# Optimization experiments

Hardware: AMD Instinct MI355X
Metric: run time of the kernel (lower is better)

## Reference

```python
import jax, jax.numpy as jnp
import numpy as np

EPS = 1e-8
UNTANH = 0.5                       # hp UNTANH (blend factor, assumed)
BUNTANH_SCALE = (2.0 + 2.0 ** 0.5) ** 0.5  # sqrt(2 + sqrt(2)) from source
C_MOMENT = 0.99                    # hp c_moment
A_VARIANCE = 0.02                  # hp a_variance
SINKHORN_ITERS = 8


def rms_norm(x, axes):
    ms = jnp.mean(x * x, axis=axes, keepdims=True)
    return x * jax.lax.rsqrt(ms + EPS)


def buntanh(x):
    # blended un-tanh: untanh * identity + (1-untanh) * tanh, rescaled
    return BUNTANH_SCALE * (UNTANH * x + (1.0 - UNTANH) * jnp.tanh(x))


def sinkhorn_knopp(A, n_iter=SINKHORN_ITERS):
    A = jnp.maximum(A, 0.0) + EPS
    def body(A, _):
        A = A / jnp.sum(A, axis=-1, keepdims=True)  # row normalize
        A = A / jnp.sum(A, axis=-2, keepdims=True)  # col normalize
        return A, None
    A, _ = jax.lax.scan(body, A, None, length=n_iter)
    return A


def setup_inputs() -> dict:
    key = jax.random.key(0)
    ks = jax.random.split(key, 8)
    B, N, D, IN_DIM = 4, 1024, 128, 8192
    inv_sqrt_d = 1.0 / np.sqrt(D)
    return {
        "state": jax.random.normal(ks[0], (B, N, D), jnp.float32) * 0.1,
        "output": jax.random.normal(ks[1], (B, N, D), jnp.float32) * 0.1,
        "w1": jax.random.normal(ks[2], (B, N, D, D), jnp.float32) * inv_sqrt_d,
        "w2": jax.random.normal(ks[3], (B, N, D, D), jnp.float32) * inv_sqrt_d,
        "w3": jax.random.normal(ks[4], (B, N, D, D), jnp.float32) * inv_sqrt_d,
        "A_ema": jax.random.normal(ks[5], (B, N, N), jnp.float32) * 0.01,
        "env_input": jax.random.normal(ks[6], (B, IN_DIM), jnp.float32),
        "noise": jax.random.normal(ks[7], (B, N, D), jnp.float32),
    }


def reference(state, output, w1, w2, w3, A_ema, env_input, noise):
    B, N, D = state.shape
    input_dim = env_input.shape[1]
    num_in = -(-input_dim // D)  # ceil

    # first-call mask/EMA adjustment (num_input_nodes change branch)
    A_mask = jnp.ones((N, N), dtype=state.dtype).at[:num_in, :].set(0.0)
    A_ema = A_ema.at[:, num_in, :num_in].add(3.0 / num_in)

    # per-node batched small GEMMs + custom activation
    Q = buntanh(jnp.einsum('bnd,bndk->bnk', state, w3))
    K = buntanh(jnp.einsum('bnd,bndk->bnk', state, w2))
    prediction = buntanh(jnp.einsum('bnd,bndk->bnk', state, w1))

    # QK^T adjacency, rms-normed over full [N,N]
    raw_A = jnp.einsum('bnk,bmk->bnm', Q, K) / jnp.sqrt(jnp.asarray(D, state.dtype))
    raw_A = rms_norm(raw_A, (-2, -1))

    # EMA (non-first step) + input-node masking
    new_A_ema = (A_ema * C_MOMENT + raw_A * (1.0 - C_MOMENT)) * A_mask

    # doubly-stochastic projection, thresholded sparsification, re-project
    dsA = sinkhorn_knopp(new_A_ema)
    baseline = 1.0 / (N + 1.0)
    sparse_A = jnp.where(dsA > baseline, dsA, 0.0)
    A = sinkhorn_knopp(sparse_A) * A_mask

    # boredom noise scaled by variance deficit (torch var is unbiased)
    var = jnp.var(A, axis=(-2, -1), keepdims=True, ddof=1)
    vd = jax.nn.relu(A_VARIANCE - var)
    V = output + vd * noise

    # message passing + softsign, overwrite input-node rows with env input
    target = jax.nn.soft_sign(jnp.einsum('bnm,bmd->bnd', A, V))
    pad = num_in * D - input_dim
    env = jnp.pad(env_input, ((0, 0), (0, pad))).reshape(B, num_in, D)
    target = target.at[:, :num_in, :].set(env)

    out = jnp.concatenate([target, prediction], axis=-1)  # [B,N,2D]
    return out, A
```

## Files before the change

kernel.cpp:

```cpp
#include <hip/hip_runtime.h>
#include <math.h>

#define NB 4
#define NN 1024
#define ND 128
#define NUM_IN 64
#define F_EPS 1e-8f
#define BT_SCALE 1.8477590650225735f
#define INV_SQRT_D 0.08838834764831844f
#define BASELINE (1.0f/1025.0f)
#define OUT_STRIDE 256
#define A_OFF 1048576

__device__ __forceinline__ float buntanh_f(float x) {
    return BT_SCALE * (0.5f * x + 0.5f * tanhf(x));
}
__device__ __forceinline__ float wave_sum(float v) {
    #pragma unroll
    for (int off = 32; off > 0; off >>= 1) v += __shfl_xor(v, off, 64);
    return v;
}
__device__ __forceinline__ float bflo(unsigned u) { return __uint_as_float(u << 16); }
__device__ __forceinline__ float bfhi(unsigned u) { return __uint_as_float(u & 0xffff0000u); }
__device__ __forceinline__ unsigned bf_rne(float f) {
    unsigned x = __float_as_uint(f);
    return (x + 0x7fffu + ((x >> 16) & 1u)) >> 16;
}
__device__ __forceinline__ unsigned bf_pack(float lo, float hi) {
    return bf_rne(lo) | (bf_rne(hi) << 16);
}

typedef float f32x4 __attribute__((ext_vector_type(4)));
__device__ __forceinline__ float4 ntload4(const float4* p) {
    f32x4 v = __builtin_nontemporal_load((const f32x4*)p);
    return make_float4(v.x, v.y, v.z, v.w);
}

__global__ __launch_bounds__(256, 6) void qkp_kernel(
    const float* __restrict__ state,
    const float* __restrict__ w1,
    const float* __restrict__ w2,
    const float* __restrict__ w3,
    float* __restrict__ dout,
    float* __restrict__ Qg,
    float* __restrict__ Kg)
{
    const int blk = blockIdx.x;
    const int node = ((blk & 7) << 9) | (blk >> 3);

    __shared__ float s_state[ND];
    __shared__ float4 red[3][8][32];

    const int t = threadIdx.x;
    if (t < 32) ((float4*)s_state)[t] =
        ((const float4*)(state + ((size_t)node << 7)))[t];
    __syncthreads();

    const int g = t >> 5, m = t & 31;

    auto do_mat = [&](const float* wbase, int q) {
        const float4* w4 = (const float4*)(wbase + ((size_t)node << 14));
        float4 wv[8];
        float4 acc = make_float4(0.f, 0.f, 0.f, 0.f);
        #pragma unroll
        for (int i = 0; i < 8; ++i) wv[i] = ntload4(&w4[i*256 + t]);
        #pragma unroll
        for (int i = 0; i < 8; ++i) {
            const float s = s_state[i*8 + g];
            acc.x += s*wv[i].x; acc.y += s*wv[i].y;
            acc.z += s*wv[i].z; acc.w += s*wv[i].w;
        }
        #pragma unroll
        for (int i = 0; i < 8; ++i) wv[i] = ntload4(&w4[(8+i)*256 + t]);
        #pragma unroll
        for (int i = 0; i < 8; ++i) {
            const float s = s_state[(8+i)*8 + g];
            acc.x += s*wv[i].x; acc.y += s*wv[i].y;
            acc.z += s*wv[i].z; acc.w += s*wv[i].w;
        }
        red[q][g][m] = acc;
    };
    do_mat(w1, 0);
    do_mat(w2, 1);
    do_mat(w3, 2);
    __syncthreads();

    if (t < 96) {
        const int q = t >> 5, mm = t & 31;
        float4 o = red[q][0][mm];
        #pragma unroll
        for (int gg = 1; gg < 8; ++gg) {
            const float4 r = red[q][gg][mm];
            o.x += r.x; o.y += r.y; o.z += r.z; o.w += r.w;
        }
        o.x = buntanh_f(o.x); o.y = buntanh_f(o.y);
        o.z = buntanh_f(o.z); o.w = buntanh_f(o.w);
        if (q == 0) {
            *(float4*)(dout + (size_t)node * OUT_STRIDE + ND + 4*mm) = o;
        } else {
            float* base = (q == 1) ? Kg : Qg;
            *(float4*)(base + ((size_t)node << 7) + 4*mm) = o;
        }
    }
}

__global__ __launch_bounds__(256) void qk2_kernel(
    const float* __restrict__ Qg, const float* __restrict__ Kg,
    unsigned* __restrict__ rawbf, float* __restrict__ reds)
{
    const int b = blockIdx.x >> 10;
    const int tile = blockIdx.x & 1023;
    const int tr = tile >> 5, tc = tile & 31;

    __shared__ float Qs[32][132];
    __shared__ float Ks[32][136];
    __shared__ float wr4[4];

    const int t = threadIdx.x;
    for (int i = t; i < 1024; i += 256) {
        const int r = i >> 5, q = i & 31;
        *(float4*)&Qs[r][q*4] = *(const float4*)(Qg + (((size_t)(b*NN + tr*32 + r)) << 7) + q*4);
        *(float4*)&Ks[r][q*4] = *(const float4*)(Kg + (((size_t)(b*NN + tc*32 + r)) << 7) + q*4);
    }
    __syncthreads();

    const int ty = t >> 4;
    const int tx = t & 15;
    float a00=0.f, a01=0.f, a10=0.f, a11=0.f;
    #pragma unroll
    for (int dq = 0; dq < 32; ++dq) {
        const float4 q0 = *(const float4*)&Qs[ty][dq*4];
        const float4 q1 = *(const float4*)&Qs[ty+16][dq*4];
        const float4 k0 = *(const float4*)&Ks[2*tx][dq*4];
        const float4 k1 = *(const float4*)&Ks[2*tx+1][dq*4];
        a00 += q0.x*k0.x + q0.y*k0.y + q0.z*k0.z + q0.w*k0.w;
        a01 += q0.x*k1.x + q0.y*k1.y + q0.z*k1.z + q0.w*k1.w;
        a10 += q1.x*k0.x + q1.y*k0.y + q1.z*k0.z + q1.w*k0.w;
        a11 += q1.x*k1.x + q1.y*k1.y + q1.z*k1.z + q1.w*k1.w;
    }
    a00 *= INV_SQRT_D; a01 *= INV_SQRT_D; a10 *= INV_SQRT_D; a11 *= INV_SQRT_D;

    unsigned* r0p = rawbf + (((size_t)(b*NN + tr*32 + ty)) << 9) + tc*16;
    unsigned* r1p = rawbf + (((size_t)(b*NN + tr*32 + ty + 16)) << 9) + tc*16;
    r0p[tx] = bf_pack(a00, a01);
    r1p[tx] = bf_pack(a10, a11);

    float ssq = a00*a00 + a01*a01 + a10*a10 + a11*a11;
    ssq = wave_sum(ssq);
    if ((t & 63) == 0) wr4[t >> 6] = ssq;
    __syncthreads();
    if (t == 0) atomicAdd(&reds[b], wr4[0]+wr4[1]+wr4[2]+wr4[3]);
}

__global__ __launch_bounds__(256) void emaT_kernel(
    const unsigned* __restrict__ rawbf, const float* __restrict__ A_ema,
    const float* __restrict__ reds,
    unsigned* __restrict__ M0, unsigned* __restrict__ M0T,
    float* __restrict__ SR)
{
    const int b = blockIdx.x >> 8;
    const int tile = blockIdx.x & 255;
    const int tr = tile >> 4, tc = tile & 15;
    const int R0 = tr << 6, C0 = tc << 6;

    __shared__ float st[64][65];
    __shared__ float s_part[64][5];

    const int t = threadIdx.x;
    const int r = t >> 2, q = t & 3;
    const int row = R0 + r;
    const float scale = rsqrtf(reds[b] * (1.0f/1048576.0f) + F_EPS);

    const unsigned* rawrow = rawbf + (((size_t)(b*NN + row)) << 9) + tc*8*4;
    const uint4 u0 = ((const uint4*)rawrow)[q*2];
    const uint4 u1 = ((const uint4*)rawrow)[q*2 + 1];
    float rv[16];
    rv[0]=bflo(u0.x); rv[1]=bfhi(u0.x); rv[2]=bflo(u0.y); rv[3]=bfhi(u0.y);
    rv[4]=bflo(u0.z); rv[5]=bfhi(u0.z); rv[6]=bflo(u0.w); rv[7]=bfhi(u0.w);
    rv[8]=bflo(u1.x); rv[9]=bfhi(u1.x); rv[10]=bflo(u1.y); rv[11]=bfhi(u1.y);
    rv[12]=bflo(u1.z); rv[13]=bfhi(u1.z); rv[14]=bflo(u1.w); rv[15]=bfhi(u1.w);

    const float* emarow = A_ema + (((size_t)(b*NN + row)) << 10) + C0 + q*16;
    float s = 0.f;
    #pragma unroll
    for (int j = 0; j < 4; ++j) {
        const float4 e = ((const float4*)emarow)[j];
        float ev[4] = {e.x, e.y, e.z, e.w};
        #pragma unroll
        for (int k = 0; k < 4; ++k) {
            const int e_idx = j*4 + k;
            const int c = C0 + q*16 + e_idx;
            float em = ev[k];
            if (row == NUM_IN && c < NUM_IN) em += 3.0f / NUM_IN;
            float v = em * 0.99f + rv[e_idx] * scale * 0.01f;
            if (row < NUM_IN) v = 0.f;
            v = fmaxf(v, 0.f) + F_EPS;
            rv[e_idx] = v;
            st[r][q*16 + e_idx] = v;
            s += v;
        }
    }
    s_part[r][q] = s;

    unsigned* m0row = M0 + (((size_t)(b*NN + row)) << 9) + tc*8*4;
    uint4 o0, o1;
    o0.x = bf_pack(rv[0],rv[1]);  o0.y = bf_pack(rv[2],rv[3]);
    o0.z = bf_pack(rv[4],rv[5]);  o0.w = bf_pack(rv[6],rv[7]);
    o1.x = bf_pack(rv[8],rv[9]);  o1.y = bf_pack(rv[10],rv[11]);
    o1.z = bf_pack(rv[12],rv[13]); o1.w = bf_pack(rv[14],rv[15]);
    ((uint4*)m0row)[q*2]     = o0;
    ((uint4*)m0row)[q*2 + 1] = o1;
    __syncthreads();

    if (t < 64) {
        const float rs = s_part[t][0] + s_part[t][1] + s_part[t][2] + s_part[t][3];
        atomicAdd(&SR[b*NN + R0 + t], rs);
    }

    const int cT = t >> 2;
    float tv[16];
    #pragma unroll
    for (int k = 0; k < 16; ++k) tv[k] = st[q*16 + k][cT];
    uint4 w0, w1;
    w0.x = bf_pack(tv[0],tv[1]);  w0.y = bf_pack(tv[2],tv[3]);
    w0.z = bf_pack(tv[4],tv[5]);  w0.w = bf_pack(tv[6],tv[7]);
    w1.x = bf_pack(tv[8],tv[9]);  w1.y = bf_pack(tv[10],tv[11]);
    w1.z = bf_pack(tv[12],tv[13]); w1.w = bf_pack(tv[14],tv[15]);
    unsigned* mtrow = M0T + (((size_t)(b*NN + C0 + cT)) << 9) + tr*8*4;
    ((uint4*)mtrow)[q*2]     = w0;
    ((uint4*)mtrow)[q*2 + 1] = w1;
}

template<bool INV_IN>
__global__ __launch_bounds__(256) void mv_kernel(
    const unsigned* __restrict__ Abf, const float* __restrict__ x,
    float* __restrict__ y)
{
    const int blk = blockIdx.x;
    const int lp  = ((blk & 7) << 5) | (blk >> 3);
    const int b   = lp >> 6;
    const int r0  = (lp & 63) << 4;
    const int t = threadIdx.x;
    const int w = t >> 6, l = t & 63;

    const float4* xb = (const float4*)(x + (b << 10));
    float4 x0 = xb[2*l], x1 = xb[2*l+1], x2 = xb[128+2*l], x3 = xb[129+2*l];
    if (INV_IN) {
        x0.x=1.f/x0.x; x0.y=1.f/x0.y; x0.z=1.f/x0.z; x0.w=1.f/x0.w;
        x1.x=1.f/x1.x; x1.y=1.f/x1.y; x1.z=1.f/x1.z; x1.w=1.f/x1.w;
        x2.x=1.f/x2.x; x2.y=1.f/x2.y; x2.z=1.f/x2.z; x2.w=1.f/x2.w;
        x3.x=1.f/x3.x; x3.y=1.f/x3.y; x3.z=1.f/x3.z; x3.w=1.f/x3.w;
    }

    #pragma unroll
    for (int r = 0; r < 4; ++r) {
        const int row = r0 + (w << 2) + r;
        const unsigned* rp = Abf + (((size_t)((b << 10) + row)) << 9);
        const uint4 v0 = ((const uint4*)rp)[l];
        const uint4 v1 = ((const uint4*)rp)[64 + l];
        float a = bflo(v0.x)*x0.x + bfhi(v0.x)*x0.y
                + bflo(v0.y)*x0.z + bfhi(v0.y)*x0.w
                + bflo(v0.z)*x1.x + bfhi(v0.z)*x1.y
                + bflo(v0.w)*x1.z + bfhi(v0.w)*x1.w
                + bflo(v1.x)*x2.x + bfhi(v1.x)*x2.y
                + bflo(v1.y)*x2.z + bfhi(v1.y)*x2.w
                + bflo(v1.z)*x3.x + bfhi(v1.z)*x3.y
                + bflo(v1.w)*x3.z + bfhi(v1.w)*x3.w;
        a = wave_sum(a);
        if (l == 0) y[(b << 10) + row] = 1.0f / a;
    }
}

__global__ __launch_bounds__(256) void thresh_kernel(
    const unsigned* __restrict__ M0, const unsigned* __restrict__ M0T,
    const float* __restrict__ r8, const float* __restrict__ c8,
    unsigned* __restrict__ A1, unsigned* __restrict__ A1T,
    float* __restrict__ SR2)
{
    const int t = threadIdx.x;
    const int b = blockIdx.x >> 6;
    const int g0 = (blockIdx.x & 63) << 4;
    const int w = t >> 6, l = t & 63;
    const bool doA1 = (w < 2);
    const int wr = doA1 ? w : (w - 2);
    const unsigned* src = doA1 ? M0 : M0T;
    unsigned*       dst = doA1 ? A1 : A1T;
    const float* rowS = doA1 ? r8 : c8;
    const float* colS = doA1 ? c8 : r8;

    const float4* cb = (const float4*)(colS + (b << 10));
    const float4 c0 = cb[2*l], c1 = cb[2*l+1], c2 = cb[128+2*l], c3 = cb[129+2*l];
    const float cm[16] = {c0.x,c0.y,c0.z,c0.w, c1.x,c1.y,c1.z,c1.w,
                          c2.x,c2.y,c2.z,c2.w, c3.x,c3.y,c3.z,c3.w};

    for (int rr = 0; rr < 8; ++rr) {
        const int row = g0 + wr*8 + rr;
        const float ri = rowS[(b << 10) + row];
        const unsigned* rp = src + (((size_t)(b*NN + row)) << 9);
        const uint4 v0 = ((const uint4*)rp)[l];
        const uint4 v1 = ((const uint4*)rp)[64 + l];
        float e[16];
        e[0]=bflo(v0.x); e[1]=bfhi(v0.x); e[2]=bflo(v0.y); e[3]=bfhi(v0.y);
        e[4]=bflo(v0.z); e[5]=bfhi(v0.z); e[6]=bflo(v0.w); e[7]=bfhi(v0.w);
        e[8]=bflo(v1.x); e[9]=bfhi(v1.x); e[10]=bflo(v1.y); e[11]=bfhi(v1.y);
        e[12]=bflo(v1.z); e[13]=bfhi(v1.z); e[14]=bflo(v1.w); e[15]=bfhi(v1.w);
        float s = 0.f;
        #pragma unroll
        for (int j = 0; j < 16; ++j) {
            const float d = e[j] * ri * cm[j];
            e[j] = (d > BASELINE ? d : 0.f) + F_EPS;
            s += e[j];
        }
        uint4 o0, o1;
        o0.x = bf_pack(e[0],e[1]);  o0.y = bf_pack(e[2],e[3]);
        o0.z = bf_pack(e[4],e[5]);  o0.w = bf_pack(e[6],e[7]);
        o1.x = bf_pack(e[8],e[9]);  o1.y = bf_pack(e[10],e[11]);
        o1.z = bf_pack(e[12],e[13]); o1.w = bf_pack(e[14],e[15]);
        unsigned* op = dst + (((size_t)(b*NN + row)) << 9);
        ((uint4*)op)[l] = o0;
        ((uint4*)op)[64 + l] = o1;
        if (doA1) {
            s = wave_sum(s);
            if (l == 0) SR2[b*NN + row] = s;
        }
    }
}

__global__ __launch_bounds__(256) void fin_kernel(
    const unsigned* __restrict__ A1, const float* __restrict__ r8,
    const float* __restrict__ c8, float* __restrict__ reds,
    float* __restrict__ dout)
{
    __shared__ float wred[8];
    const int t = threadIdx.x;
    const int b = blockIdx.x >> 6;
    const int g0 = (blockIdx.x & 63) << 4;
    const int w = t >> 6, l = t & 63;

    const float4* cb = (const float4*)(c8 + (b << 10));
    const float4 c0 = cb[2*l], c1 = cb[2*l+1], c2 = cb[128+2*l], c3 = cb[129+2*l];
    const float cm[16] = {c0.x,c0.y,c0.z,c0.w, c1.x,c1.y,c1.z,c1.w,
                          c2.x,c2.y,c2.z,c2.w, c3.x,c3.y,c3.z,c3.w};

    float s1 = 0.f, s2 = 0.f;
    for (int rr = 0; rr < 4; ++rr) {
        const int row = g0 + w*4 + rr;
        float* Arow = dout + A_OFF + (((size_t)(b*NN + row)) << 10);
        if (row < NUM_IN) {
            const float4 z = make_float4(0.f,0.f,0.f,0.f);
            ((float4*)Arow)[2*l] = z;       ((float4*)Arow)[2*l+1] = z;
            ((float4*)Arow)[128+2*l] = z;   ((float4*)Arow)[129+2*l] = z;
        } else {
            const float ri = r8[(b << 10) + row];
            const unsigned* rp = A1 + (((size_t)(b*NN + row)) << 9);
            const uint4 v0 = ((const uint4*)rp)[l];
            const uint4 v1 = ((const uint4*)rp)[64 + l];
            float e[16];
            e[0]=bflo(v0.x); e[1]=bfhi(v0.x); e[2]=bflo(v0.y); e[3]=bfhi(v0.y);
            e[4]=bflo(v0.z); e[5]=bfhi(v0.z); e[6]=bflo(v0.w); e[7]=bfhi(v0.w);
            e[8]=bflo(v1.x); e[9]=bfhi(v1.x); e[10]=bflo(v1.y); e[11]=bfhi(v1.y);
            e[12]=bflo(v1.z); e[13]=bfhi(v1.z); e[14]=bflo(v1.w); e[15]=bfhi(v1.w);
            #pragma unroll
            for (int j = 0; j < 16; ++j) {
                e[j] = e[j] * ri * cm[j];
                s1 += e[j]; s2 += e[j]*e[j];
            }
            ((float4*)Arow)[2*l]     = make_float4(e[0],e[1],e[2],e[3]);
            ((float4*)Arow)[2*l+1]   = make_float4(e[4],e[5],e[6],e[7]);
            ((float4*)Arow)[128+2*l] = make_float4(e[8],e[9],e[10],e[11]);
            ((float4*)Arow)[129+2*l] = make_float4(e[12],e[13],e[14],e[15]);
        }
    }
    s1 = wave_sum(s1); s2 = wave_sum(s2);
    if (l == 0) { wred[w] = s1; wred[4 + w] = s2; }
    __syncthreads();
    if (t == 0) {
        atomicAdd(&reds[4 + b], wred[0]+wred[1]+wred[2]+wred[3]);
        atomicAdd(&reds[8 + b], wred[4]+wred[5]+wred[6]+wred[7]);
    }
}

__global__ __launch_bounds__(256) void vbuild_kernel(
    const float* __restrict__ outp, const float* __restrict__ noise,
    const float* __restrict__ reds, float* __restrict__ V)
{
    const int i = blockIdx.x * 256 + threadIdx.x;
    const int b = i >> 15;
    const float Mn = 1048576.f;
    const float S1 = reds[4 + b], S2 = reds[8 + b];
    const float var = (S2 - S1*S1/Mn) / (Mn - 1.f);
    const float vd = fmaxf(0.02f - var, 0.f);
    const float4 o = ((const float4*)outp)[i];
    const float4 n = ((const float4*)noise)[i];
    ((float4*)V)[i] = make_float4(o.x + vd*n.x, o.y + vd*n.y,
                                  o.z + vd*n.z, o.w + vd*n.w);
}

__global__ __launch_bounds__(256) void av_kernel(
    const float* __restrict__ A,
    const float* __restrict__ V,
    const float* __restrict__ env,
    float* __restrict__ dout)
{
    const int b = blockIdx.x >> 5;
    const int rb = blockIdx.x & 31;
    const int r0 = rb << 5;
    const int t = threadIdx.x;

    if (r0 < NUM_IN) {
        for (int i = t; i < 32 * ND; i += 256) {
            const int r = i >> 7, d = i & 127;
            dout[((size_t)(b*NN + r0 + r)) * OUT_STRIDE + d] =
                env[(size_t)b * 8192 + (size_t)(r0 + r) * ND + d];
        }
        return;
    }

    __shared__ float As[32][64];
    const int d = t & 127, rg = t >> 7;
    float acc[16];
    #pragma unroll
    for (int k = 0; k < 16; ++k) acc[k] = 0.f;
    const float* Vb = V + (size_t)b * (NN * ND) + d;

    for (int mc = 0; mc < 16; ++mc) {
        #pragma unroll
        for (int j = 0; j < 2; ++j) {
            const int f = 2*t + j, r = f >> 4, c4 = f & 15;
            *(float4*)&As[r][c4*4] =
                *(const float4*)(A + (((size_t)(b*NN + r0 + r)) << 10) + mc*64 + c4*4);
        }
        __syncthreads();
        #pragma unroll 4
        for (int mm4 = 0; mm4 < 16; ++mm4) {
            const float vv0 = Vb[(size_t)(mc*64 + mm4*4 + 0) * ND];
            const float vv1 = Vb[(size_t)(mc*64 + mm4*4 + 1) * ND];
            const float vv2 = Vb[(size_t)(mc*64 + mm4*4 + 2) * ND];
            const float vv3 = Vb[(size_t)(mc*64 + mm4*4 + 3) * ND];
            #pragma unroll
            for (int k = 0; k < 16; ++k) {
                const float4 a = *(const float4*)&As[rg*16 + k][mm4*4];
                acc[k] += a.x*vv0 + a.y*vv1 + a.z*vv2 + a.w*vv3;
            }
        }
        __syncthreads();
    }
    #pragma unroll
    for (int k = 0; k < 16; ++k) {
        const float o = acc[k];
        dout[((size_t)(b*NN + r0 + rg*16 + k)) * OUT_STRIDE + d] = o / (1.f + fabsf(o));
    }
}

extern "C" void kernel_launch(void* const* d_in, const int* in_sizes, int n_in,
                              void* d_out, int out_size, void* d_ws, size_t ws_size,
                              hipStream_t stream)
{
    (void)in_sizes; (void)n_in; (void)out_size; (void)ws_size;
    const float* state = (const float*)d_in[0];
    const float* outp  = (const float*)d_in[1];
    const float* w1    = (const float*)d_in[2];
    const float* w2    = (const float*)d_in[3];
    const float* w3    = (const float*)d_in[4];
    const float* A_ema = (const float*)d_in[5];
    const float* env   = (const float*)d_in[6];
    const float* noise = (const float*)d_in[7];
    float* dout = (float*)d_out;

    unsigned* M0  = (unsigned*)(dout + A_OFF);
    unsigned* M0T = M0 + 2097152;

    float*    Qg   = (float*)d_ws;
    float*    Kg   = Qg + 524288;
    float*    Vg   = Kg + 524288;
    unsigned* raw  = (unsigned*)(Vg + 524288);
    unsigned* A1   = raw;
    unsigned* A1T  = raw + 2097152;
    float*    SR1  = (float*)(A1T + 2097152);
    float*    reds = SR1 + 4096;
    float*    SC1  = reds + 16;
    float*    SR2  = SC1 + 4096;
    float*    SC2  = SR2 + 4096;
    float*    RV1  = SC2 + 4096;
    float*    RV2  = RV1 + 4096;

    hipMemsetAsync(SR1, 0, (4096 + 16) * sizeof(float), stream);

    qkp_kernel<<<dim3(NB*NN), dim3(256), 0, stream>>>(
        state, w1, w2, w3, dout, Qg, Kg);

    qk2_kernel<<<dim3(NB*1024), dim3(256), 0, stream>>>(Qg, Kg, raw, reds);

    emaT_kernel<<<dim3(NB*256), dim3(256), 0, stream>>>(
        raw, A_ema, reds, M0, M0T, SR1);

    mv_kernel<true ><<<dim3(256), dim3(256), 0, stream>>>(M0T, SR1, SC1);
    for (int k = 1; k < 15; ++k) {
        if (k & 1)
            mv_kernel<false><<<dim3(256), dim3(256), 0, stream>>>(M0, SC1, RV1);
        else
            mv_kernel<false><<<dim3(256), dim3(256), 0, stream>>>(M0T, RV1, SC1);
    }

    thresh_kernel<<<dim3(NB*64), dim3(256), 0, stream>>>(
        M0, M0T, RV1, SC1, A1, A1T, SR2);

    mv_kernel<true ><<<dim3(256), dim3(256), 0, stream>>>(A1T, SR2, SC2);
    for (int k = 1; k < 15; ++k) {
        if (k & 1)
            mv_kernel<false><<<dim3(256), dim3(256), 0, stream>>>(A1, SC2, RV2);
        else
            mv_kernel<false><<<dim3(256), dim3(256), 0, stream>>>(A1T, RV2, SC2);
    }

    fin_kernel<<<dim3(NB*64), dim3(256), 0, stream>>>(A1, RV2, SC2, reds, dout);

    vbuild_kernel<<<dim3(512), dim3(256), 0, stream>>>(outp, noise, reds, Vg);

    av_kernel<<<dim3(NB*32), dim3(256), 0, stream>>>(dout + A_OFF, Vg, env, dout);
}
```

Baseline: 503.0 us.

## Split A·V matmul across K into partial sums with separate reduction kernel

```diff
diff --git a/kernel.cpp b/kernel.cpp
--- a/kernel.cpp
+++ b/kernel.cpp
@@ -396,60 +396,65 @@
                                   o.z + vd*n.z, o.w + vd*n.w);
 }
 
-__global__ __launch_bounds__(256) void av_kernel(
+__global__ __launch_bounds__(256) void av_part(
     const float* __restrict__ A,
     const float* __restrict__ V,
-    const float* __restrict__ env,
+    float* __restrict__ P)
+{
+    const int bid = blockIdx.x;
+    const int ks = bid & 3;
+    const int rt = (bid >> 2) % 60;
+    const int b  = bid / 240;
+    const int r0 = NUM_IN + rt * 16;
+    const int mc0 = ks << 8;
+    const int t = threadIdx.x;
+    const int d = t & 127, rg = t >> 7;
+    const int rowb = r0 + rg*8;
+
+    float acc[8] = {0.f,0.f,0.f,0.f,0.f,0.f,0.f,0.f};
+    const float* Vb = V + ((size_t)b << 17) + ((size_t)mc0 << 7) + d;
+    const float* Ab = A + (((size_t)(b*NN + rowb)) << 10) + mc0;
+
+    #pragma unroll 4
+    for (int mq = 0; mq < 64; ++mq) {
+        const float v0 = Vb[(mq*4 + 0) << 7];
+        const float v1 = Vb[(mq*4 + 1) << 7];
+        const float v2 = Vb[(mq*4 + 2) << 7];
+        const float v3 = Vb[(mq*4 + 3) << 7];
+        #pragma unroll
+        for (int k = 0; k < 8; ++k) {
+            const float4 a = *(const float4*)(Ab + ((size_t)k << 10) + mq*4);
+            acc[k] += a.x*v0 + a.y*v1 + a.z*v2 + a.w*v3;
+        }
+    }
+    #pragma unroll
+    for (int k = 0; k < 8; ++k) {
+        const int ridx = rt*16 + rg*8 + k;
+        P[(((size_t)(ks*NB + b)) * 960 + ridx) * 128 + d] = acc[k];
+    }
+}
+
+__global__ __launch_bounds__(256) void av_fin(
+    const float* __restrict__ P, const float* __restrict__ env,
     float* __restrict__ dout)
 {
-    const int b = blockIdx.x >> 5;
-    const int rb = blockIdx.x & 31;
-    const int r0 = rb << 5;
-    const int t = threadIdx.x;
-
-    if (r0 < NUM_IN) {
-        for (int i = t; i < 32 * ND; i += 256) {
-            const int r = i >> 7, d = i & 127;
-            dout[((size_t)(b*NN + r0 + r)) * OUT_STRIDE + d] =
-                env[(size_t)b * 8192 + (size_t)(r0 + r) * ND + d];
-        }
+    const int t = threadIdx.x;
+    int bid = blockIdx.x;
+    if (bid < 128) {
+        const int idx = bid*256 + t;
+        const int b = idx >> 13, off = idx & 8191;
+        const int r = off >> 7, d = off & 127;
+        dout[((size_t)(b*NN + r)) * OUT_STRIDE + d] = env[idx];
         return;
     }
-
-    __shared__ float As[32][64];
-    const int d = t & 127, rg = t >> 7;
-    float acc[16];
-    #pragma unroll
-    for (int k = 0; k < 16; ++k) acc[k] = 0.f;
-    const float* Vb = V + (size_t)b * (NN * ND) + d;
-
-    for (int mc = 0; mc < 16; ++mc) {
-        #pragma unroll
-        for (int j = 0; j < 2; ++j) {
-            const int f = 2*t + j, r = f >> 4, c4 = f & 15;
-            *(float4*)&As[r][c4*4] =
-                *(const float4*)(A + (((size_t)(b*NN + r0 + r)) << 10) + mc*64 + c4*4);
-        }
-        __syncthreads();
-        #pragma unroll 4
-        for (int mm4 = 0; mm4 < 16; ++mm4) {
-            const float vv0 = Vb[(size_t)(mc*64 + mm4*4 + 0) * ND];
-            const float vv1 = Vb[(size_t)(mc*64 + mm4*4 + 1) * ND];
-            const float vv2 = Vb[(size_t)(mc*64 + mm4*4 + 2) * ND];
-            const float vv3 = Vb[(size_t)(mc*64 + mm4*4 + 3) * ND];
-            #pragma unroll
-            for (int k = 0; k < 16; ++k) {
-                const float4 a = *(const float4*)&As[rg*16 + k][mm4*4];
-                acc[k] += a.x*vv0 + a.y*vv1 + a.z*vv2 + a.w*vv3;
-            }
-        }
-        __syncthreads();
-    }
-    #pragma unroll
-    for (int k = 0; k < 16; ++k) {
-        const float o = acc[k];
-        dout[((size_t)(b*NN + r0 + rg*16 + k)) * OUT_STRIDE + d] = o / (1.f + fabsf(o));
-    }
+    bid -= 128;
+    const int idx = bid*256 + t;
+    const int d = idx & 127;
+    const int rd = idx >> 7;
+    const int b = rd / 960;
+    const int ridx = rd - b*960;
+    const float s = P[idx] + P[idx + 491520] + P[idx + 2*491520] + P[idx + 3*491520];
+    dout[((size_t)(b*NN + NUM_IN + ridx)) * OUT_STRIDE + d] = s / (1.f + fabsf(s));
 }
 
 extern "C" void kernel_launch(void* const* d_in, const int* in_sizes, int n_in,
@@ -476,6 +481,7 @@
     unsigned* raw  = (unsigned*)(Vg + 524288);
     unsigned* A1   = raw;
     unsigned* A1T  = raw + 2097152;
+    float*    Pp   = (float*)A1T;
     float*    SR1  = (float*)(A1T + 2097152);
     float*    reds = SR1 + 4096;
     float*    SC1  = reds + 16;
@@ -517,5 +523,7 @@
 
     vbuild_kernel<<<dim3(512), dim3(256), 0, stream>>>(outp, noise, reds, Vg);
 
-    av_kernel<<<dim3(NB*32), dim3(256), 0, stream>>>(dout + A_OFF, Vg, env, dout);
-}
+    av_part<<<dim3(960), dim3(256), 0, stream>>>(dout + A_OFF, Vg, Pp);
+
+    av_fin<<<dim3(2048), dim3(256), 0, stream>>>(Pp, env, dout);
+}
```

Result: faster. 422.1 us (-16.1%).
